# Kernel tuning notes

Hardware: AMD Instinct MI355X
Metric: run time of the kernel (lower is better)

## Reference

```python
import jax, jax.numpy as jnp
import numpy as np

K, PAD, STRIDE, TREE_DEPTH = 3, 1, 1, 3


def _unfold(x, k, pad, stride):
    # torch.nn.Unfold, channel-major feature ordering: feat = c*k*k + (ki*k+kj)
    B, C, H, W = x.shape
    Ho = (H + 2 * pad - k) // stride + 1
    Wo = (W + 2 * pad - k) // stride + 1
    xp = jnp.pad(x, ((0, 0), (0, 0), (pad, pad), (pad, pad)))
    cols = [xp[:, :, ki:ki + stride * Ho:stride, kj:kj + stride * Wo:stride]
            for ki in range(k) for kj in range(k)]
    p = jnp.stack(cols, axis=2)               # [B, C, k*k, Ho, Wo]
    p = p.reshape(B, C * k * k, Ho * Wo)      # [B, C*k*k, L]
    return p.transpose(0, 2, 1), Ho, Wo       # [B, L, C*k*k]


def _bin_ops(a, b):
    # the 16 soft binary logic gates, stacked on a trailing axis
    ab = a * b
    s = a + b
    zero = jnp.zeros_like(a)
    one = jnp.ones_like(a)
    return jnp.stack([zero, ab, a - ab, a, b - ab, b,
                      s - 2 * ab, s - ab, 1 - (s - ab), 1 - (s - 2 * ab),
                      1 - b, 1 - b + ab, 1 - a, 1 - a + ab, 1 - ab, one], axis=-1)


def setup_inputs() -> dict:
    key = jax.random.key(0)
    k1, k2 = jax.random.split(key)
    B, C_in, H, W = 16, 64, 32, 32
    C_out = 128
    x = jax.random.uniform(k1, (B, C_in, H, W), dtype=jnp.float32)
    weights = jax.random.normal(k2, (C_out, 2 ** TREE_DEPTH - 1, 16), dtype=jnp.float32)
    # replicate the module's leaf-index construction: 2 random channels,
    # 4 random spatial taps each, flattened as c*patch_size + spatial
    rng = np.random.default_rng(0)
    idx = []
    for _ in range(C_out):
        chans = rng.permutation(C_in)[:2]
        parts = [c * (K * K) + rng.permutation(K * K)[:2 ** TREE_DEPTH // 2] for c in chans]
        idx.append(np.concatenate(parts))
    leaf_indices = jnp.asarray(np.stack(idx), dtype=jnp.int32)  # [C_out, 8]
    return {"x": x, "weights": weights, "leaf_indices": leaf_indices}


def reference(x, weights, leaf_indices):
    patches, Ho, Wo = _unfold(x, K, PAD, STRIDE)          # [B, L, C*9]
    # gather the 8 leaf inputs for every output channel at once
    leaves = jnp.take(patches, leaf_indices, axis=2)      # [B, L, O, 8]
    cur = leaves
    for level in range(TREE_DEPTH):
        npairs = cur.shape[-1] // 2
        # faithful to source: gate_idx = 2**level - 1 + pair (indices overlap across levels)
        gate_ids = 2 ** level - 1 + jnp.arange(npairs)
        w = jax.nn.softmax(weights[:, gate_ids], axis=-1)  # [O, npairs, 16]
        a = cur[..., 0::2]
        b = cur[..., 1::2]
        ops = _bin_ops(a, b)                               # [B, L, O, npairs, 16]
        cur = jnp.einsum('blopg,opg->blop', ops, w)        # [B, L, O, npairs]
    out = cur[..., 0]                                      # [B, L, O]
    B = x.shape[0]
    return out.transpose(0, 2, 1).reshape(B, weights.shape[0], Ho, Wo)
```

## Files before the change

### kernel.cpp

```cpp
#include <hip/hip_runtime.h>


#define C_OUT 128
#define C_IN  64
#define HW    32

__device__ __forceinline__ float4 ld4u(const float* p) {
    float4 v;
    __builtin_memcpy(&v, p, sizeof(float4));
    return v;
}

__device__ __forceinline__ float4 gate4(const float4 c, const float4 a, const float4 b) {
    float4 r;
    r.x = fmaf(a.x * b.x, c.w, fmaf(a.x, c.y, fmaf(b.x, c.z, c.x)));
    r.y = fmaf(a.y * b.y, c.w, fmaf(a.y, c.y, fmaf(b.y, c.z, c.x)));
    r.z = fmaf(a.z * b.z, c.w, fmaf(a.z, c.y, fmaf(b.z, c.z, c.x)));
    r.w = fmaf(a.w * b.w, c.w, fmaf(a.w, c.y, fmaf(b.w, c.z, c.x)));
    return r;
}

__global__ __launch_bounds__(256) void logic_tree_fused(
    const float* __restrict__ x, const float* __restrict__ wts,
    const int* __restrict__ leaf_idx, float* __restrict__ out)
{
    const int blk = blockIdx.x;
    const int b = blk >> 7;
    const int o = blk & (C_OUT - 1);

    __shared__ float4 cf_s[4];
    if (threadIdx.x < 4) {
        const int g = threadIdx.x;
        const float* wp = wts + (o * 7 + g) * 16;
        float v[16];
        float m = -1e30f;
        #pragma unroll
        for (int i = 0; i < 16; ++i) { v[i] = wp[i]; m = fmaxf(m, v[i]); }
        float s = 0.f;
        #pragma unroll
        for (int i = 0; i < 16; ++i) { v[i] = expf(v[i] - m); s += v[i]; }
        float inv = 1.f / s;
        #pragma unroll
        for (int i = 0; i < 16; ++i) v[i] *= inv;
        float c0  = v[8]+v[9]+v[10]+v[11]+v[12]+v[13]+v[14]+v[15];
        float ca  = v[2]+v[3]+v[6]+v[7]-v[8]-v[9]-v[12]-v[13];
        float cb  = v[4]+v[5]+v[6]+v[7]-v[8]-v[9]-v[10]-v[11];
        float cab = v[1]-v[2]-v[4]-2.f*v[6]-v[7]+v[8]+2.f*v[9]+v[11]+v[13]-v[14];
        cf_s[g] = make_float4(c0, ca, cb, cab);
    }

    int cch[8], dy[8], dxx[8];
    #pragma unroll
    for (int j = 0; j < 8; ++j) {
        int li = leaf_idx[o * 8 + j];
        int c = li / 9;
        int kk = li - c * 9;
        int ky = kk / 3;
        cch[j] = c; dy[j] = ky - 1; dxx[j] = (kk - ky * 3) - 1;
    }
    __syncthreads();

    const int q = threadIdx.x & 7;
    const int h = threadIdx.x >> 3;
    const float* xb = x + (size_t)b * C_IN * HW * HW;

    float4 v[8];
    #pragma unroll
    for (int j = 0; j < 8; ++j) {
        int hh = h + dy[j];
        bool hok = ((unsigned)hh < HW);
        const float* rp = xb + (cch[j] * HW + (hok ? hh : 0)) * HW;
        float4 t;
        if (dxx[j] == 0) {
            t = ld4u(rp + 4 * q);
        } else {
            int base = 4 * q + dxx[j];
            int cb = min(max(base, 0), HW - 4);
            float4 u = ld4u(rp + cb);
            if (base < 0)            t = make_float4(0.f, u.x, u.y, u.z);
            else if (base > HW - 4)  t = make_float4(u.y, u.z, u.w, 0.f);
            else                     t = u;
        }
        if (!hok) t = make_float4(0.f, 0.f, 0.f, 0.f);
        v[j] = t;
    }

    const float4 cf0 = cf_s[0], cf1 = cf_s[1], cf2 = cf_s[2], cf3 = cf_s[3];
    float4 p0 = gate4(cf0, v[0], v[1]);
    float4 p1 = gate4(cf1, v[2], v[3]);
    float4 p2 = gate4(cf2, v[4], v[5]);
    float4 p3 = gate4(cf3, v[6], v[7]);
    float4 q0 = gate4(cf1, p0, p1);
    float4 q1 = gate4(cf2, p2, p3);
    float4 r  = gate4(cf3, q0, q1);

    float4* op = (float4*)(out + (size_t)(b * C_OUT + o) * (HW * HW));
    op[threadIdx.x] = r;
}

extern "C" void kernel_launch(void* const* d_in, const int* in_sizes, int n_in,
                              void* d_out, int out_size, void* d_ws, size_t ws_size,
                              hipStream_t stream) {
    const float* x       = (const float*)d_in[0];
    const float* weights = (const float*)d_in[1];
    const int*   leaves  = (const int*)d_in[2];
    float* out = (float*)d_out;
    logic_tree_fused<<<16 * C_OUT, 256, 0, stream>>>(x, weights, leaves, out);
}
```

Baseline: 68.71 us.

## Process eight pixels per thread with aligned loads and lane shuffles for halo

Each thread now computes eight contiguous output pixels instead of four, with 128 threads per block. The unaligned, clamped float4 loads are replaced by two aligned float4 loads per leaf, and the left and right neighbour values come from adjacent lanes via shuffles. Leaf loads are interleaved with the gate evaluation to keep fewer values live. This is meant to remove misaligned and redundant memory accesses, but it halves the thread count and raises per-thread register use.

```diff
diff --git a/kernel.cpp b/kernel.cpp
--- a/kernel.cpp
+++ b/kernel.cpp
@@ -5,22 +5,42 @@
 #define C_IN  64
 #define HW    32
 
-__device__ __forceinline__ float4 ld4u(const float* p) {
-    float4 v;
-    __builtin_memcpy(&v, p, sizeof(float4));
-    return v;
+__device__ __forceinline__ void gate8(const float4 c, const float* a,
+                                      const float* b, float* r) {
+    #pragma unroll
+    for (int i = 0; i < 8; ++i)
+        r[i] = fmaf(a[i] * b[i], c.w, fmaf(a[i], c.y, fmaf(b[i], c.z, c.x)));
 }
 
-__device__ __forceinline__ float4 gate4(const float4 c, const float4 a, const float4 b) {
-    float4 r;
-    r.x = fmaf(a.x * b.x, c.w, fmaf(a.x, c.y, fmaf(b.x, c.z, c.x)));
-    r.y = fmaf(a.y * b.y, c.w, fmaf(a.y, c.y, fmaf(b.y, c.z, c.x)));
-    r.z = fmaf(a.z * b.z, c.w, fmaf(a.z, c.y, fmaf(b.z, c.z, c.x)));
-    r.w = fmaf(a.w * b.w, c.w, fmaf(a.w, c.y, fmaf(b.w, c.z, c.x)));
-    return r;
+__device__ __forceinline__ void load_leaf(const float* __restrict__ xb,
+                                          int c, int dy, int dx,
+                                          int h, int q, float* t) {
+    int hh = h + dy;
+    bool hok = ((unsigned)hh < HW);
+    const float* rp = xb + (c * HW + (hok ? hh : 0)) * HW + 8 * q;
+    float4 e0 = *(const float4*)rp;
+    float4 e1 = *(const float4*)(rp + 4);
+    float prev = __shfl_up(e1.w, 1);
+    float next = __shfl_down(e0.x, 1);
+    float e[8] = {e0.x, e0.y, e0.z, e0.w, e1.x, e1.y, e1.z, e1.w};
+    float s[8];
+    if (dx == 0) {
+        #pragma unroll
+        for (int i = 0; i < 8; ++i) s[i] = e[i];
+    } else if (dx < 0) {
+        s[0] = (q > 0) ? prev : 0.f;
+        #pragma unroll
+        for (int i = 1; i < 8; ++i) s[i] = e[i - 1];
+    } else {
+        #pragma unroll
+        for (int i = 0; i < 7; ++i) s[i] = e[i + 1];
+        s[7] = (q < 3) ? next : 0.f;
+    }
+    #pragma unroll
+    for (int i = 0; i < 8; ++i) t[i] = hok ? s[i] : 0.f;
 }
 
-__global__ __launch_bounds__(256) void logic_tree_fused(
+__global__ __launch_bounds__(128) void logic_tree_fused(
     const float* __restrict__ x, const float* __restrict__ wts,
     const int* __restrict__ leaf_idx, float* __restrict__ out)
 {
@@ -60,42 +80,32 @@
     }
     __syncthreads();
 
-    const int q = threadIdx.x & 7;
-    const int h = threadIdx.x >> 3;
+    const int q = threadIdx.x & 3;
+    const int h = threadIdx.x >> 2;
     const float* xb = x + (size_t)b * C_IN * HW * HW;
 
-    float4 v[8];
-    #pragma unroll
-    for (int j = 0; j < 8; ++j) {
-        int hh = h + dy[j];
-        bool hok = ((unsigned)hh < HW);
-        const float* rp = xb + (cch[j] * HW + (hok ? hh : 0)) * HW;
-        float4 t;
-        if (dxx[j] == 0) {
-            t = ld4u(rp + 4 * q);
-        } else {
-            int base = 4 * q + dxx[j];
-            int cb = min(max(base, 0), HW - 4);
-            float4 u = ld4u(rp + cb);
-            if (base < 0)            t = make_float4(0.f, u.x, u.y, u.z);
-            else if (base > HW - 4)  t = make_float4(u.y, u.z, u.w, 0.f);
-            else                     t = u;
-        }
-        if (!hok) t = make_float4(0.f, 0.f, 0.f, 0.f);
-        v[j] = t;
-    }
+    const float4 cf0 = cf_s[0], cf1 = cf_s[1], cf2 = cf_s[2], cf3 = cf_s[3];
+    float la[8], lb[8], p0[8], p1[8], q0[8], q1[8], r[8];
 
-    const float4 cf0 = cf_s[0], cf1 = cf_s[1], cf2 = cf_s[2], cf3 = cf_s[3];
-    float4 p0 = gate4(cf0, v[0], v[1]);
-    float4 p1 = gate4(cf1, v[2], v[3]);
-    float4 p2 = gate4(cf2, v[4], v[5]);
-    float4 p3 = gate4(cf3, v[6], v[7]);
-    float4 q0 = gate4(cf1, p0, p1);
-    float4 q1 = gate4(cf2, p2, p3);
-    float4 r  = gate4(cf3, q0, q1);
+    load_leaf(xb, cch[0], dy[0], dxx[0], h, q, la);
+    load_leaf(xb, cch[1], dy[1], dxx[1], h, q, lb);
+    gate8(cf0, la, lb, p0);
+    load_leaf(xb, cch[2], dy[2], dxx[2], h, q, la);
+    load_leaf(xb, cch[3], dy[3], dxx[3], h, q, lb);
+    gate8(cf1, la, lb, p1);
+    gate8(cf1, p0, p1, q0);
+    load_leaf(xb, cch[4], dy[4], dxx[4], h, q, la);
+    load_leaf(xb, cch[5], dy[5], dxx[5], h, q, lb);
+    gate8(cf2, la, lb, p0);
+    load_leaf(xb, cch[6], dy[6], dxx[6], h, q, la);
+    load_leaf(xb, cch[7], dy[7], dxx[7], h, q, lb);
+    gate8(cf3, la, lb, p1);
+    gate8(cf2, p0, p1, q1);
+    gate8(cf3, q0, q1, r);
 
-    float4* op = (float4*)(out + (size_t)(b * C_OUT + o) * (HW * HW));
-    op[threadIdx.x] = r;
+    float4* op = (float4*)(out + (size_t)blk * (HW * HW) + h * HW + 8 * q);
+    op[0] = make_float4(r[0], r[1], r[2], r[3]);
+    op[1] = make_float4(r[4], r[5], r[6], r[7]);
 }
 
 extern "C" void kernel_launch(void* const* d_in, const int* in_sizes, int n_in,
@@ -105,5 +115,5 @@
     const float* weights = (const float*)d_in[1];
     const int*   leaves  = (const int*)d_in[2];
     float* out = (float*)d_out;
-    logic_tree_fused<<<16 * C_OUT, 256, 0, stream>>>(x, weights, leaves, out);
+    logic_tree_fused<<<16 * C_OUT, 128, 0, stream>>>(x, weights, leaves, out);
 }
```

Result: faster. 65.04 us (-5.3%).
